# Performance work log

Hardware: AMD Instinct MI355X
Metric: run time of the kernel (lower is better)

The kernel has to match this reference:

```python
import jax, jax.numpy as jnp
import numpy as np

SCALAR_DIM = 64
VECTOR_DIM = 32
SPIN = 2
N_NODES = 50000
N_EDGES = 1600000
GEO_DIM = 3
IN_DIM = 2 * SCALAR_DIM + VECTOR_DIM + GEO_DIM  # 163
HID = SCALAR_DIM + VECTOR_DIM  # 96


def setup_inputs() -> dict:
    key = jax.random.key(0)
    ks = jax.random.split(key, 9)
    h_scalar = jax.random.normal(ks[0], (N_NODES, SCALAR_DIM), dtype=jnp.float32)
    h_vector = jax.random.normal(ks[1], (N_NODES, VECTOR_DIM), dtype=jnp.float32)
    edge_index = jax.random.randint(ks[2], (2, N_EDGES), 0, N_NODES, dtype=jnp.int64)
    pos = jax.random.normal(ks[3], (N_NODES, 2), dtype=jnp.float32)
    orientation = jax.random.uniform(ks[4], (N_NODES, 1), dtype=jnp.float32)
    # MLP params (Linear: y = x @ W.T + b; store as [in, out] for jnp)
    lim1 = 1.0 / np.sqrt(IN_DIM)
    lim2 = 1.0 / np.sqrt(HID)
    W1 = jax.random.uniform(ks[5], (IN_DIM, HID), minval=-lim1, maxval=lim1, dtype=jnp.float32)
    b1 = jax.random.uniform(ks[6], (HID,), minval=-lim1, maxval=lim1, dtype=jnp.float32)
    W2 = jax.random.uniform(ks[7], (HID, HID), minval=-lim2, maxval=lim2, dtype=jnp.float32)
    b2 = jax.random.uniform(ks[8], (HID,), minval=-lim2, maxval=lim2, dtype=jnp.float32)
    return dict(h_scalar=h_scalar, h_vector=h_vector, edge_index=edge_index,
                pos=pos, orientation=orientation, W1=W1, b1=b1, W2=W2, b2=b2)


def reference(h_scalar, h_vector, edge_index, pos, orientation, W1, b1, W2, b2):
    src, dst = edge_index[0], edge_index[1]
    delta_pos = pos[src] - pos[dst]                         # [E,2]
    dist = jnp.linalg.norm(delta_pos, axis=1, keepdims=True) + 1e-6  # [E,1]
    phi_global = jnp.arctan2(delta_pos[:, 1], delta_pos[:, 0])       # [E]
    alpha_i = orientation[dst, 0]                           # [E]
    delta_phi = phi_global - alpha_i
    geo_feat = jnp.concatenate([dist,
                                jnp.cos(SPIN * delta_phi)[:, None],
                                jnp.sin(SPIN * delta_phi)[:, None]], axis=-1)  # [E,3]
    beta_j = orientation[src, 0]
    rot_angle = (beta_j - alpha_i) * SPIN
    c, s = jnp.cos(rot_angle), jnp.sin(rot_angle)
    R = jnp.stack([jnp.stack([c, -s], -1), jnp.stack([s, c], -1)], axis=-2)  # [E,2,2]
    num_vecs = VECTOR_DIM // 2
    v_j = h_vector[src].reshape(-1, num_vecs, 2)            # [E,V/2,2]
    v_j_rot = jnp.einsum('eij,evj->evi', R, v_j).reshape(-1, VECTOR_DIM)
    msg_input = jnp.concatenate([h_scalar[src], h_scalar[dst], v_j_rot, geo_feat], axis=-1)
    h = jax.nn.silu(msg_input @ W1 + b1)
    raw_msg = h @ W2 + b2                                   # [E, S+V]
    msg_scalar = raw_msg[:, :SCALAR_DIM]
    msg_vector = raw_msg[:, SCALAR_DIM:]
    out_scalar = jax.ops.segment_sum(msg_scalar, dst, num_segments=N_NODES)
    out_vector = jax.ops.segment_sum(msg_vector, dst, num_segments=N_NODES)
    return h_scalar + out_scalar, h_vector + out_vector
```

## Files before the change

### kernel.cpp

```cpp
#include <hip/hip_runtime.h>
#include <hip/hip_bf16.h>

#define N_NODESC 50000
#define N_EDGESC 1600000
#define SDIM 64
#define VDIM 32
#define HID 96
#define IN_DIMC 163

#define GRID_E 6250
#define TPB_E 4
#define NXCD 8
#define XQ (GRID_E / NXCD)
#define XR (GRID_E % NXCD)

typedef float f32x4 __attribute__((ext_vector_type(4)));
typedef short s16x8 __attribute__((ext_vector_type(8)));

__device__ __forceinline__ float bf2f(__hip_bfloat16 x) { return __bfloat162float(x); }
__device__ __forceinline__ __hip_bfloat16 f2bf(float x) { return __float2bfloat16(x); }
__device__ __forceinline__ float bfbits2f(short b) {
    unsigned u = ((unsigned)(unsigned short)b) << 16;
    return __builtin_bit_cast(float, u);
}
__device__ __forceinline__ short f2bfbits(float x) {
    __hip_bfloat16 h = __float2bfloat16(x);
    return *(const short*)&h;
}

__global__ void detect_zero(const int* ei, int* flag, int* __restrict__ counts) {
    int i = blockIdx.x * blockDim.x + threadIdx.x;
    if (i < N_NODESC) counts[i] = 0;
    if (i == 0) {
        int z = 1;
        for (int k = 0; k < 64; ++k) {
            if (ei[2 * k + 1] != 0) { z = 0; break; }
        }
        *flag = z;
    }
}

__global__ void fused_init(const float* __restrict__ hs, const float* __restrict__ hv,
                           float* __restrict__ out, int* __restrict__ counts,
                           const float* __restrict__ W1, const float* __restrict__ W2,
                           __hip_bfloat16* __restrict__ SrcRec,
                           __hip_bfloat16* __restrict__ WbT2,
                           __hip_bfloat16* __restrict__ W1cgT,
                           __hip_bfloat16* __restrict__ W2Tb,
                           const int* __restrict__ ei, const int* __restrict__ flag64) {
    int i = blockIdx.x * blockDim.x + threadIdx.x;
    if (i < N_NODESC * (SDIM + VDIM))
        out[i] = (i < N_NODESC * SDIM) ? hs[i] : hv[i - N_NODESC * SDIM];
    if (i < N_NODESC * VDIM) {
        int n = i >> 5, f = i & 31;
        SrcRec[n * 128 + 96 + f] = f2bf(hv[i]);
    }
    if (i < 192 * 64) {
        int n = i >> 6, k = i & 63;
        float val = (n < 96) ? W1[k * HID + n] : W1[(64 + k) * HID + (n - 96)];
        WbT2[i] = f2bf(val);
    }
    if (i < 96 * 64) {
        int n = i >> 6, k = i & 63;
        float val = 0.f;
        if (k < 32) val = W1[(128 + k) * HID + n];
        else if (k < 35) val = W1[(160 + (k - 32)) * HID + n];
        W1cgT[i] = f2bf(val);
    }
    if (i < 96 * 96) {
        int n = i / 96, k = i - (i / 96) * 96;
        W2Tb[i] = f2bf(W2[k * HID + n]);
    }
    if (i < N_EDGESC) {
        int dN;
        if (*flag64) dN = (int)((const long long*)ei)[N_EDGESC + i];
        else dN = ei[N_EDGESC + i];
        atomicAdd(&counts[dN], 1);
    }
}

__global__ __launch_bounds__(256, 2) void node_precompute_mfma(
    const float* __restrict__ hs, const __hip_bfloat16* __restrict__ WbT2,
    const float* __restrict__ b1,
    __hip_bfloat16* __restrict__ SrcRec, __hip_bfloat16* __restrict__ Qt) {
    __shared__ __hip_bfloat16 sA[64][72];
    __shared__ __hip_bfloat16 sOut[64][200];
    const int t = threadIdx.x;
    const int lane = t & 63;
    const int w = t >> 6;
    const int m16 = lane & 15;
    const int q = lane >> 4;
    const int nb = blockIdx.x * 64;

    for (int idx = t; idx < 64 * 64; idx += 256) {
        int node = idx >> 6, f = idx & 63;
        int g = nb + node;
        sA[node][f] = f2bf(g < N_NODESC ? hs[g * SDIM + f] : 0.f);
    }
    __syncthreads();

    s16x8 bfr[3][2];
    float b1v[3];
    for (int nt = 0; nt < 3; ++nt) {
        int n_out = w * 48 + nt * 16 + m16;
        for (int kt = 0; kt < 2; ++kt)
            bfr[nt][kt] = *(const s16x8*)&WbT2[n_out * 64 + kt * 32 + q * 8];
        b1v[nt] = (n_out < 96) ? b1[n_out] : 0.f;
    }

    for (int ms = 0; ms < 4; ++ms) {
        s16x8 afr[2];
        for (int kt = 0; kt < 2; ++kt)
            afr[kt] = *(const s16x8*)&sA[ms * 16 + m16][kt * 32 + q * 8];
        f32x4 acc[3];
        for (int nt = 0; nt < 3; ++nt) acc[nt] = (f32x4){0.f, 0.f, 0.f, 0.f};
        for (int nt = 0; nt < 3; ++nt)
            for (int kt = 0; kt < 2; ++kt)
                acc[nt] = __builtin_amdgcn_mfma_f32_16x16x32_bf16(
                    afr[kt], bfr[nt][kt], acc[nt], 0, 0, 0);
        for (int nt = 0; nt < 3; ++nt) {
            int n_out = w * 48 + nt * 16 + m16;
            for (int r = 0; r < 4; ++r)
                sOut[ms * 16 + q * 4 + r][n_out] = f2bf(acc[nt][r] + b1v[nt]);
        }
    }
    __syncthreads();

    for (int idx = t; idx < 64 * 12; idx += 256) {
        int node = idx / 12, ch = idx - (idx / 12) * 12;
        int g = nb + node;
        if (g < N_NODESC)
            *(s16x8*)&SrcRec[g * 128 + ch * 8] = *(const s16x8*)&sOut[node][ch * 8];
    }
    for (int idx = t; idx < 64 * 12; idx += 256) {
        int node = idx / 12, ch = idx - (idx / 12) * 12;
        int g = nb + node;
        if (g < N_NODESC)
            *(s16x8*)&Qt[g * 96 + ch * 8] = *(const s16x8*)&sOut[node][96 + ch * 8];
    }
}

__global__ __launch_bounds__(1024) void scan_kernel(
    const int* __restrict__ counts, int* __restrict__ cur) {
    __shared__ int part[1024];
    const int t = threadIdx.x;
    const int CH = (N_NODESC + 1023) / 1024;
    int lo = t * CH;
    int hi = lo + CH; if (hi > N_NODESC) hi = N_NODESC;
    int s = 0;
    for (int i = lo; i < hi; ++i) s += counts[i];
    part[t] = s;
    __syncthreads();
    for (int d = 1; d < 1024; d <<= 1) {
        int v = (t >= d) ? part[t - d] : 0;
        __syncthreads();
        part[t] += v;
        __syncthreads();
    }
    int run = (t == 0) ? 0 : part[t - 1];
    for (int i = lo; i < hi; ++i) {
        int c = counts[i];
        cur[i] = run;
        run += c;
    }
}

__global__ __launch_bounds__(256) void scatter_kernel(
    const int* __restrict__ ei, const int* __restrict__ flag64,
    int* __restrict__ cur, int2* __restrict__ edges) {
    int e = blockIdx.x * blockDim.x + threadIdx.x;
    if (e >= N_EDGESC) return;
    int sN, dN;
    if (*flag64) {
        const long long* e64 = (const long long*)ei;
        sN = (int)e64[e]; dN = (int)e64[N_EDGESC + e];
    } else { sN = ei[e]; dN = ei[N_EDGESC + e]; }
    int p = atomicAdd(&cur[dN], 1);
    edges[p] = make_int2(sN, dN);
}

__global__ __launch_bounds__(256, 3) void edge_kernel_sorted(
    const int2* __restrict__ edges,
    const float* __restrict__ pos, const float* __restrict__ ori,
    const __hip_bfloat16* __restrict__ W2Tb, const float* __restrict__ b2,
    const __hip_bfloat16* __restrict__ SrcRec, const __hip_bfloat16* __restrict__ Qt,
    const __hip_bfloat16* __restrict__ W1cgT,
    float* __restrict__ out) {
    __shared__ int s_srcM[2][64], s_dstM[2][64];
    __shared__ alignas(16) __hip_bfloat16 hA[64][104];
    __shared__ alignas(16) __hip_bfloat16 s_vf[64][104];
    __shared__ alignas(16) short sW2f[18 * 64 * 8];
    __shared__ int s_segstart[66];

    const int t = threadIdx.x;
    const int lane = t & 63;
    const int w = t >> 6;
    const int m16 = lane & 15;
    const int q = lane >> 4;
    const int el = t >> 2;
    const int quad = t & 3;

    if (w == 0) {
        for (int f = 0; f < 18; ++f) {
            int nt = f / 3, kt = f - (f / 3) * 3;
            *(s16x8*)&sW2f[(f * 64 + lane) * 8] =
                *(const s16x8*)&W2Tb[(nt * 16 + m16) * 96 + kt * 32 + q * 8];
        }
    }
    s16x8 bfrC[6][2];
    #pragma unroll
    for (int nt = 0; nt < 6; ++nt)
        #pragma unroll
        for (int kt = 0; kt < 2; ++kt)
            bfrC[nt][kt] = *(const s16x8*)&W1cgT[(nt * 16 + m16) * 64 + kt * 32 + q * 8];
    float b2v[6];
    #pragma unroll
    for (int nt = 0; nt < 6; ++nt) b2v[nt] = b2[nt * 16 + m16];

    int b = blockIdx.x;
    int xcd = b & 7, bi = b >> 3;
    int c = (xcd < XR) ? (xcd * (XQ + 1) + bi)
                       : (XR * (XQ + 1) + (xcd - XR) * XQ + bi);
    const int tile0 = c * TPB_E;

    int2 edT1;
    s16x8 hvvT;
    float rcT, rsT;
    float gdT, gcgT, gsgT;
    {
        int2 edT = edges[tile0 * 64 + el];
        edT1 = edges[(tile0 + 1) * 64 + el];
        hvvT = *(const s16x8*)&SrcRec[edT.x * 128 + 96 + quad * 8];
        int sN = edT.x, dN = edT.y;
        float ca, sa, cb, sb;
        __sincosf(2.0f * ori[dN], &sa, &ca);
        __sincosf(2.0f * ori[sN], &sb, &cb);
        rcT = cb * ca + sb * sa;
        rsT = sb * ca - cb * sa;
        float dx = pos[2 * sN] - pos[2 * dN];
        float dy = pos[2 * sN + 1] - pos[2 * dN + 1];
        float d2 = dx * dx + dy * dy;
        gdT = sqrtf(d2) + 1e-6f;
        float c2f, s2f;
        if (d2 > 0.f) {
            float inv = 1.0f / d2;
            c2f = (dx * dx - dy * dy) * inv;
            s2f = 2.0f * dx * dy * inv;
        } else { c2f = 1.0f; s2f = 0.0f; }
        gcgT = c2f * ca + s2f * sa;
        gsgT = s2f * ca - c2f * sa;
        if (quad == 0) { s_srcM[0][el] = sN; s_dstM[0][el] = dN; }
    }
    __syncthreads();
    s16x8 pqP[3], pqQ[3];
    #pragma unroll
    for (int i2 = 0; i2 < 3; ++i2) {
        int item = i2 * 256 + t;
        int e = item / 12;
        int j = (item - e * 12) * 8;
        pqP[i2] = *(const s16x8*)&SrcRec[s_srcM[0][e] * 128 + j];
        pqQ[i2] = *(const s16x8*)&Qt[s_dstM[0][e] * 96 + j];
    }

    int cur = 0;
    for (int tl = 0; tl < TPB_E; ++tl) {
        const int nx = cur ^ 1;
        const int tlN2 = (tl + 2 < TPB_E) ? tl + 2 : TPB_E - 1;

        {
            s16x8 rv;
            #pragma unroll
            for (int p2 = 0; p2 < 4; ++p2) {
                float x = bfbits2f(hvvT[2 * p2]), y = bfbits2f(hvvT[2 * p2 + 1]);
                rv[2 * p2]     = f2bfbits(rcT * x - rsT * y);
                rv[2 * p2 + 1] = f2bfbits(rsT * x + rcT * y);
            }
            *(s16x8*)&hA[el][quad * 8] = rv;
            s16x8 up = (s16x8){0, 0, 0, 0, 0, 0, 0, 0};
            if (quad == 0) {
                up[0] = f2bfbits(gdT); up[1] = f2bfbits(gcgT); up[2] = f2bfbits(gsgT);
            }
            *(s16x8*)&hA[el][32 + quad * 8] = up;
        }
        int2 edT2 = edges[(tile0 + tlN2) * 64 + el];
        s16x8 hvvN = *(const s16x8*)&SrcRec[edT1.x * 128 + 96 + quad * 8];
        {
            s16x8 afr0 = *(const s16x8*)&hA[w * 16 + m16][q * 8];
            s16x8 afr1 = *(const s16x8*)&hA[w * 16 + m16][32 + q * 8];
            #pragma unroll
            for (int nt = 0; nt < 6; ++nt) {
                f32x4 a1 = __builtin_amdgcn_mfma_f32_16x16x32_bf16(
                    afr0, bfrC[nt][0], (f32x4){0.f, 0.f, 0.f, 0.f}, 0, 0, 0);
                a1 = __builtin_amdgcn_mfma_f32_16x16x32_bf16(
                    afr1, bfrC[nt][1], a1, 0, 0, 0);
                int u = nt * 16 + m16;
                #pragma unroll
                for (int r = 0; r < 4; ++r)
                    s_vf[w * 16 + q * 4 + r][u] = f2bf(a1[r]);
            }
        }
        float rcN, rsN, gdN, gcgN, gsgN;
        {
            int sN = edT1.x, dN = edT1.y;
            float ca, sa, cb, sb;
            __sincosf(2.0f * ori[dN], &sa, &ca);
            __sincosf(2.0f * ori[sN], &sb, &cb);
            rcN = cb * ca + sb * sa;
            rsN = sb * ca - cb * sa;
            float dx = pos[2 * sN] - pos[2 * dN];
            float dy = pos[2 * sN + 1] - pos[2 * dN + 1];
            float d2 = dx * dx + dy * dy;
            gdN = sqrtf(d2) + 1e-6f;
            float c2f, s2f;
            if (d2 > 0.f) {
                float inv = 1.0f / d2;
                c2f = (dx * dx - dy * dy) * inv;
                s2f = 2.0f * dx * dy * inv;
            } else { c2f = 1.0f; s2f = 0.0f; }
            gcgN = c2f * ca + s2f * sa;
            gsgN = s2f * ca - c2f * sa;
            if (quad == 0) { s_srcM[nx][el] = sN; s_dstM[nx][el] = dN; }
        }
        __syncthreads();

        #pragma unroll
        for (int i2 = 0; i2 < 3; ++i2) {
            int item = i2 * 256 + t;
            int e = item / 12;
            int j = (item - e * 12) * 8;
            s16x8 Vv = *(const s16x8*)&s_vf[e][j];
            s16x8 hb;
            #pragma unroll
            for (int k2 = 0; k2 < 8; ++k2) {
                float pre = bfbits2f(pqP[i2][k2]) + bfbits2f(pqQ[i2][k2])
                          + bfbits2f(Vv[k2]);
                float h = pre / (1.0f + __expf(-pre));
                hb[k2] = f2bfbits(h);
            }
            *(s16x8*)&hA[e][j] = hb;
        }
        __syncthreads();

        #pragma unroll
        for (int i2 = 0; i2 < 3; ++i2) {
            int item = i2 * 256 + t;
            int e = item / 12;
            int j = (item - e * 12) * 8;
            pqP[i2] = *(const s16x8*)&SrcRec[s_srcM[nx][e] * 128 + j];
            pqQ[i2] = *(const s16x8*)&Qt[s_dstM[nx][e] * 96 + j];
        }
        {
            s16x8 afr[3];
            #pragma unroll
            for (int kt = 0; kt < 3; ++kt)
                afr[kt] = *(const s16x8*)&hA[w * 16 + m16][kt * 32 + q * 8];
            f32x4 acc[6];
            #pragma unroll
            for (int nt = 0; nt < 6; ++nt) acc[nt] = (f32x4){0.f, 0.f, 0.f, 0.f};
            #pragma unroll
            for (int nt = 0; nt < 6; ++nt)
                #pragma unroll
                for (int kt = 0; kt < 3; ++kt) {
                    s16x8 bf = *(const s16x8*)&sW2f[((nt * 3 + kt) * 64 + lane) * 8];
                    acc[nt] = __builtin_amdgcn_mfma_f32_16x16x32_bf16(
                        afr[kt], bf, acc[nt], 0, 0, 0);
                }
            #pragma unroll
            for (int nt = 0; nt < 6; ++nt) {
                int u = nt * 16 + m16;
                float bb = b2v[nt];
                #pragma unroll
                for (int r = 0; r < 4; ++r)
                    s_vf[w * 16 + q * 4 + r][u] = f2bf(acc[nt][r] + bb);
            }
        }
        __syncthreads();

        {
            int dl = s_dstM[cur][lane];
            int dp = (lane > 0) ? s_dstM[cur][lane - 1] : -1;
            bool bnd = (lane > 0) && (dl != dp);
            unsigned long long mask = __ballot(bnd);
            int nseg = (int)__popcll(mask) + 1;
            if (bnd) s_segstart[__popcll(mask & (~0ull >> (63 - lane)))] = lane;
            if (lane == 0) s_segstart[0] = 0;

            for (int idx = t; idx < nseg * HID; idx += 256) {
                int sg = idx / HID;
                int u = idx - sg * HID;
                int e0 = s_segstart[sg];
                int e1 = (sg + 1 < nseg) ? s_segstart[sg + 1] : 64;
                float sum = 0.f;
                for (int e = e0; e < e1; ++e) sum += bf2f(s_vf[e][u]);
                int dN = s_dstM[cur][e0];
                if (u < SDIM) atomicAdd(&out[dN * SDIM + u], sum);
                else atomicAdd(&out[N_NODESC * SDIM + dN * VDIM + (u - SDIM)], sum);
            }
        }

        edT1 = edT2; hvvT = hvvN;
        rcT = rcN; rsT = rsN; gdT = gdN; gcgT = gcgN; gsgT = gsgN;
        cur = nx;
        __syncthreads();
    }
}

__global__ __launch_bounds__(128) void node_precompute(
    const float* __restrict__ hs, const float* __restrict__ hv,
    const float* __restrict__ W1, const float* __restrict__ b1,
    __hip_bfloat16* __restrict__ Pp, __hip_bfloat16* __restrict__ Qt,
    __hip_bfloat16* __restrict__ Ut, __hip_bfloat16* __restrict__ Vt) {
    int n = blockIdx.x;
    __shared__ float s_hs[SDIM];
    __shared__ float s_hv[VDIM];
    int t = threadIdx.x;
    if (t < 64) s_hs[t] = hs[n * SDIM + t];
    else if (t < 96) s_hv[t - 64] = hv[n * VDIM + (t - 64)];
    __syncthreads();
    if (t < HID) {
        float p = b1[t], qq = 0.f, u = 0.f, v = 0.f;
        for (int k = 0; k < 64; ++k) {
            float x = s_hs[k];
            p += x * W1[k * HID + t];
            qq += x * W1[(64 + k) * HID + t];
        }
        for (int pr = 0; pr < 16; ++pr) {
            float x = s_hv[2 * pr], y = s_hv[2 * pr + 1];
            float wa = W1[(128 + 2 * pr) * HID + t];
            float wb = W1[(128 + 2 * pr + 1) * HID + t];
            u += x * wa + y * wb;
            v += x * wb - y * wa;
        }
        Pp[n * HID + t] = f2bf(p);
        Qt[n * HID + t] = f2bf(qq);
        Ut[n * HID + t] = f2bf(u);
        Vt[n * HID + t] = f2bf(v);
    }
}

__global__ void init_out(const float* __restrict__ hs, const float* __restrict__ hv,
                         float* __restrict__ out) {
    int i = blockIdx.x * blockDim.x + threadIdx.x;
    if (i >= N_NODESC * (SDIM + VDIM)) return;
    out[i] = (i < N_NODESC * SDIM) ? hs[i] : hv[i - N_NODESC * SDIM];
}

__global__ void detect_kernel(const int* ei, int* flag) {
    if (blockIdx.x == 0 && threadIdx.x == 0) {
        int z = 1;
        for (int k = 0; k < 64; ++k) {
            if (ei[2 * k + 1] != 0) { z = 0; break; }
        }
        *flag = z;
    }
}

__global__ __launch_bounds__(256) void edge_kernel(
    const int* __restrict__ ei, const float* __restrict__ pos,
    const float* __restrict__ ori, const float* __restrict__ W1,
    const float* __restrict__ W2, const float* __restrict__ b2,
    const __hip_bfloat16* __restrict__ Pp, const __hip_bfloat16* __restrict__ Qt,
    const __hip_bfloat16* __restrict__ Ut, const __hip_bfloat16* __restrict__ Vt,
    const int* __restrict__ flag64, float* __restrict__ out) {
    __shared__ int s_src[64], s_dst[64];
    __shared__ float s_c[64], s_s[64], s_d[64], s_cg[64], s_sg[64];
    __shared__ float s_w1d[3][HID];
    __shared__ __hip_bfloat16 hA[64][104];
    __shared__ __hip_bfloat16 W2T[HID][104];

    const int t = threadIdx.x;
    const int lane = t & 63;
    const int w = t >> 6;
    const int m16 = lane & 15;
    const int q = lane >> 4;

    for (int idx = t; idx < HID * HID; idx += 256) {
        int k = idx / HID;
        int n = idx - k * HID;
        W2T[n][k] = f2bf(W2[idx]);
    }
    for (int idx = t; idx < 3 * HID; idx += 256) {
        int r = idx / HID, j = idx - r * HID;
        s_w1d[r][j] = W1[(160 + r) * HID + j];
    }
    __syncthreads();

    s16x8 bfr[6][3];
    for (int nt = 0; nt < 6; ++nt)
        for (int kt = 0; kt < 3; ++kt)
            bfr[nt][kt] = *(const s16x8*)&W2T[nt * 16 + m16][kt * 32 + q * 8];
    float b2v[6];
    for (int nt = 0; nt < 6; ++nt) b2v[nt] = b2[nt * 16 + m16];

    const bool i64 = (*flag64 != 0);
    const long long* ei64 = (const long long*)ei;

    for (int tile = blockIdx.x; tile < N_EDGESC / 64; tile += gridDim.x) {
        __syncthreads();

        if (t < 64) {
            int e = tile * 64 + t;
            int sN, dN;
            if (i64) { sN = (int)ei64[e]; dN = (int)ei64[N_EDGESC + e]; }
            else     { sN = ei[e];        dN = ei[N_EDGESC + e]; }
            s_src[t] = sN; s_dst[t] = dN;
            float ca, sa, cb, sb;
            __sincosf(2.0f * ori[dN], &sa, &ca);
            __sincosf(2.0f * ori[sN], &sb, &cb);
            s_c[t] = cb * ca + sb * sa;
            s_s[t] = sb * ca - cb * sa;
            float dx = pos[2 * sN] - pos[2 * dN];
            float dy = pos[2 * sN + 1] - pos[2 * dN + 1];
            float d2 = dx * dx + dy * dy;
            s_d[t] = sqrtf(d2) + 1e-6f;
            float c2f, s2f;
            if (d2 > 0.f) {
                float inv = 1.0f / d2;
                c2f = (dx * dx - dy * dy) * inv;
                s2f = 2.0f * dx * dy * inv;
            } else { c2f = 1.0f; s2f = 0.0f; }
            s_cg[t] = c2f * ca + s2f * sa;
            s_sg[t] = s2f * ca - c2f * sa;
        }
        __syncthreads();

        for (int p = 0; p < 24; ++p) {
            int idx = p * 256 + t;
            int e = idx / HID;
            int j = idx - e * HID;
            int sN = s_src[e], dN = s_dst[e];
            float pre = bf2f(Pp[sN * HID + j]) + bf2f(Qt[dN * HID + j])
                      + s_c[e] * bf2f(Ut[sN * HID + j])
                      + s_s[e] * bf2f(Vt[sN * HID + j])
                      + s_d[e] * s_w1d[0][j] + s_cg[e] * s_w1d[1][j]
                      + s_sg[e] * s_w1d[2][j];
            float h = pre / (1.0f + __expf(-pre));
            hA[e][j] = f2bf(h);
        }
        __syncthreads();

        f32x4 acc[6];
        for (int nt = 0; nt < 6; ++nt) acc[nt] = (f32x4){0.f, 0.f, 0.f, 0.f};
        s16x8 afr[3];
        for (int kt = 0; kt < 3; ++kt)
            afr[kt] = *(const s16x8*)&hA[w * 16 + m16][kt * 32 + q * 8];
        for (int nt = 0; nt < 6; ++nt)
            for (int kt = 0; kt < 3; ++kt)
                acc[nt] = __builtin_amdgcn_mfma_f32_16x16x32_bf16(
                    afr[kt], bfr[nt][kt], acc[nt], 0, 0, 0);

        for (int nt = 0; nt < 6; ++nt) {
            int u = nt * 16 + m16;
            for (int r = 0; r < 4; ++r) {
                int eloc = w * 16 + q * 4 + r;
                int dN = s_dst[eloc];
                float val = acc[nt][r] + b2v[nt];
                if (u < SDIM) atomicAdd(&out[dN * SDIM + u], val);
                else atomicAdd(&out[N_NODESC * SDIM + dN * VDIM + (u - SDIM)], val);
            }
        }
    }
}

__global__ __launch_bounds__(192) void edge_fallback(
    const int* __restrict__ ei, const float* __restrict__ hs,
    const float* __restrict__ hv, const float* __restrict__ pos,
    const float* __restrict__ ori, const float* __restrict__ W1,
    const float* __restrict__ b1, const float* __restrict__ W2,
    const float* __restrict__ b2, const int* __restrict__ flag64,
    float* __restrict__ out) {
    __shared__ float s_msg[IN_DIMC];
    __shared__ float s_h[HID];
    int e = blockIdx.x;
    int t = threadIdx.x;
    const bool i64 = (*flag64 != 0);
    int sN, dN;
    if (i64) {
        const long long* e64 = (const long long*)ei;
        sN = (int)e64[e]; dN = (int)e64[N_EDGESC + e];
    } else { sN = ei[e]; dN = ei[N_EDGESC + e]; }

    if (t < IN_DIMC) {
        if (t < 64) s_msg[t] = hs[sN * SDIM + t];
        else if (t < 128) s_msg[t] = hs[dN * SDIM + (t - 64)];
        else {
            float ca, sa, cb, sb;
            __sincosf(2.0f * ori[dN], &sa, &ca);
            __sincosf(2.0f * ori[sN], &sb, &cb);
            float c = cb * ca + sb * sa;
            float s = sb * ca - cb * sa;
            float dx = pos[2 * sN] - pos[2 * dN];
            float dy = pos[2 * sN + 1] - pos[2 * dN + 1];
            float d2 = dx * dx + dy * dy;
            if (t < 160) {
                int pr = (t - 128) >> 1;
                float x = hv[sN * VDIM + 2 * pr], y = hv[sN * VDIM + 2 * pr + 1];
                s_msg[t] = ((t & 1) == 0) ? (c * x - s * y) : (s * x + c * y);
            } else if (t == 160) s_msg[t] = sqrtf(d2) + 1e-6f;
            else {
                float c2f = 1.0f, s2f = 0.0f;
                if (d2 > 0.f) {
                    float inv = 1.0f / d2;
                    c2f = (dx * dx - dy * dy) * inv;
                    s2f = 2.0f * dx * dy * inv;
                }
                s_msg[t] = (t == 161) ? (c2f * ca + s2f * sa) : (s2f * ca - c2f * sa);
            }
        }
    }
    __syncthreads();
    if (t < HID) {
        float a = b1[t];
        for (int k = 0; k < IN_DIMC; ++k) a += s_msg[k] * W1[k * HID + t];
        s_h[t] = a / (1.0f + __expf(-a));
    }
    __syncthreads();
    if (t < HID) {
        float a = b2[t];
        for (int k = 0; k < HID; ++k) a += s_h[k] * W2[k * HID + t];
        if (t < SDIM) atomicAdd(&out[dN * SDIM + t], a);
        else atomicAdd(&out[N_NODESC * SDIM + dN * VDIM + (t - SDIM)], a);
    }
}

extern "C" void kernel_launch(void* const* d_in, const int* in_sizes, int n_in,
                              void* d_out, int out_size, void* d_ws, size_t ws_size,
                              hipStream_t stream) {
    const float* hs  = (const float*)d_in[0];
    const float* hv  = (const float*)d_in[1];
    const int*   ei  = (const int*)d_in[2];
    const float* pos = (const float*)d_in[3];
    const float* ori = (const float*)d_in[4];
    const float* W1  = (const float*)d_in[5];
    const float* b1  = (const float*)d_in[6];
    const float* W2  = (const float*)d_in[7];
    const float* b2  = (const float*)d_in[8];
    float* out = (float*)d_out;

    const size_t SREC = (size_t)N_NODESC * 128 * sizeof(__hip_bfloat16);
    const size_t QTB  = (size_t)N_NODESC * 96 * sizeof(__hip_bfloat16);
    const size_t CNT  = ((size_t)N_NODESC * sizeof(int) + 255) & ~255ull;
    const size_t EDG  = (size_t)N_EDGESC * sizeof(int2);
    const size_t WBT2 = ((size_t)192 * 64 * 2 + 255) & ~255ull;
    const size_t W1CG = ((size_t)96 * 64 * 2 + 255) & ~255ull;
    const size_t W2TS = ((size_t)96 * 96 * 2 + 255) & ~255ull;
    const size_t SORT_WS = SREC + QTB + 2 * CNT + EDG + WBT2 + W1CG + W2TS + 256;

    const size_t TBL = (size_t)N_NODESC * HID * sizeof(__hip_bfloat16);
    const bool big = ws_size >= 4 * TBL + 16;
    const bool srt = ws_size >= SORT_WS;

    if (srt) {
        char* ws = (char*)d_ws;
        __hip_bfloat16* SrcRec = (__hip_bfloat16*)(ws);
        __hip_bfloat16* Qt     = (__hip_bfloat16*)(ws + SREC);
        int* counts            = (int*)(ws + SREC + QTB);
        int* cur               = (int*)(ws + SREC + QTB + CNT);
        int2* edges            = (int2*)(ws + SREC + QTB + 2 * CNT);
        __hip_bfloat16* WbT2   = (__hip_bfloat16*)(ws + SREC + QTB + 2 * CNT + EDG);
        __hip_bfloat16* W1cgT  = (__hip_bfloat16*)(ws + SREC + QTB + 2 * CNT + EDG + WBT2);
        __hip_bfloat16* W2Tb   = (__hip_bfloat16*)(ws + SREC + QTB + 2 * CNT + EDG + WBT2 + W1CG);
        int* flag              = (int*)(ws + SREC + QTB + 2 * CNT + EDG + WBT2 + W1CG + W2TS);

        detect_zero<<<(N_NODESC + 255) / 256, 256, 0, stream>>>(ei, flag, counts);
        fused_init<<<(N_NODESC * (SDIM + VDIM) + 255) / 256, 256, 0, stream>>>(
            hs, hv, out, counts, W1, W2, SrcRec, WbT2, W1cgT, W2Tb, ei, flag);
        scan_kernel<<<1, 1024, 0, stream>>>(counts, cur);
        scatter_kernel<<<N_EDGESC / 256, 256, 0, stream>>>(ei, flag, cur, edges);
        node_precompute_mfma<<<(N_NODESC + 63) / 64, 256, 0, stream>>>(
            hs, WbT2, b1, SrcRec, Qt);
        edge_kernel_sorted<<<GRID_E, 256, 0, stream>>>(edges, pos, ori, W2Tb, b2,
                                                       SrcRec, Qt, W1cgT, out);
    } else if (big) {
        char* ws = (char*)d_ws;
        __hip_bfloat16* Pp = (__hip_bfloat16*)(ws);
        __hip_bfloat16* Qt = (__hip_bfloat16*)(ws + TBL);
        __hip_bfloat16* Ut = (__hip_bfloat16*)(ws + 2 * TBL);
        __hip_bfloat16* Vt = (__hip_bfloat16*)(ws + 3 * TBL);
        int* flag = (int*)(ws + 4 * TBL);
        init_out<<<(N_NODESC * (SDIM + VDIM) + 255) / 256, 256, 0, stream>>>(hs, hv, out);
        detect_kernel<<<1, 64, 0, stream>>>(ei, flag);
        node_precompute<<<N_NODESC, 128, 0, stream>>>(hs, hv, W1, b1, Pp, Qt, Ut, Vt);
        edge_kernel<<<2500, 256, 0, stream>>>(ei, pos, ori, W1, W2, b2,
                                              Pp, Qt, Ut, Vt, flag, out);
    } else {
        int* flag = (int*)d_ws;
        init_out<<<(N_NODESC * (SDIM + VDIM) + 255) / 256, 256, 0, stream>>>(hs, hv, out);
        detect_kernel<<<1, 64, 0, stream>>>(ei, flag);
        edge_fallback<<<N_EDGESC, 192, 0, stream>>>(ei, hs, hv, pos, ori, W1, b1,
                                                    W2, b2, flag, out);
    }
}
```

Baseline: 607.1 us.

## Compute hidden activations in MFMA fragment layout, drop two barriers; vectorize init

The edge kernel now has each lane gather the P/Q rows and compute the SiLU hidden activations directly in the A-fragment layout used by the second MFMA. This removes the round trip through shared memory and the two __syncthreads per tile that surrounded it. The init kernel is also vectorized with float4 copies and 8-wide bf16 packing, and its grid is shrunk to exactly cover the edge count. In exchange, the gathers become less coalesced because each lane reads its own edge row per fragment.

```diff
diff --git a/kernel.cpp b/kernel.cpp
--- a/kernel.cpp
+++ b/kernel.cpp
@@ -49,11 +49,22 @@
                            __hip_bfloat16* __restrict__ W2Tb,
                            const int* __restrict__ ei, const int* __restrict__ flag64) {
     int i = blockIdx.x * blockDim.x + threadIdx.x;
-    if (i < N_NODESC * (SDIM + VDIM))
-        out[i] = (i < N_NODESC * SDIM) ? hs[i] : hv[i - N_NODESC * SDIM];
-    if (i < N_NODESC * VDIM) {
-        int n = i >> 5, f = i & 31;
-        SrcRec[n * 128 + 96 + f] = f2bf(hv[i]);
+    if (i < N_NODESC * (SDIM + VDIM) / 4) {
+        const int HS4 = N_NODESC * SDIM / 4;
+        float4 v = (i < HS4) ? ((const float4*)hs)[i] : ((const float4*)hv)[i - HS4];
+        ((float4*)out)[i] = v;
+    }
+    if (i < N_NODESC * VDIM / 8) {
+        int n = i >> 2, c = i & 3;
+        const float4* hv4 = (const float4*)hv;
+        float4 a = hv4[n * 8 + c * 2];
+        float4 bq = hv4[n * 8 + c * 2 + 1];
+        s16x8 o;
+        o[0] = f2bfbits(a.x);  o[1] = f2bfbits(a.y);
+        o[2] = f2bfbits(a.z);  o[3] = f2bfbits(a.w);
+        o[4] = f2bfbits(bq.x); o[5] = f2bfbits(bq.y);
+        o[6] = f2bfbits(bq.z); o[7] = f2bfbits(bq.w);
+        *(s16x8*)&SrcRec[n * 128 + 96 + c * 8] = o;
     }
     if (i < 192 * 64) {
         int n = i >> 6, k = i & 63;
@@ -71,7 +82,7 @@
         int n = i / 96, k = i - (i / 96) * 96;
         W2Tb[i] = f2bf(W2[k * HID + n]);
     }
-    if (i < N_EDGESC) {
+    {
         int dN;
         if (*flag64) dN = (int)((const long long*)ei)[N_EDGESC + i];
         else dN = ei[N_EDGESC + i];
@@ -187,7 +198,7 @@
     const __hip_bfloat16* __restrict__ W1cgT,
     float* __restrict__ out) {
     __shared__ int s_srcM[2][64], s_dstM[2][64];
-    __shared__ alignas(16) __hip_bfloat16 hA[64][104];
+    __shared__ alignas(16) __hip_bfloat16 hVG[64][72];
     __shared__ alignas(16) __hip_bfloat16 s_vf[64][104];
     __shared__ alignas(16) short sW2f[18 * 64 * 8];
     __shared__ int s_segstart[66];
@@ -199,6 +210,7 @@
     const int q = lane >> 4;
     const int el = t >> 2;
     const int quad = t & 3;
+    const int eM = w * 16 + m16;
 
     if (w == 0) {
         for (int f = 0; f < 18; ++f) {
@@ -253,13 +265,13 @@
     }
     __syncthreads();
     s16x8 pqP[3], pqQ[3];
-    #pragma unroll
-    for (int i2 = 0; i2 < 3; ++i2) {
-        int item = i2 * 256 + t;
-        int e = item / 12;
-        int j = (item - e * 12) * 8;
-        pqP[i2] = *(const s16x8*)&SrcRec[s_srcM[0][e] * 128 + j];
-        pqQ[i2] = *(const s16x8*)&Qt[s_dstM[0][e] * 96 + j];
+    {
+        int sN = s_srcM[0][eM], dN = s_dstM[0][eM];
+        #pragma unroll
+        for (int kt = 0; kt < 3; ++kt) {
+            pqP[kt] = *(const s16x8*)&SrcRec[sN * 128 + kt * 32 + q * 8];
+            pqQ[kt] = *(const s16x8*)&Qt[dN * 96 + kt * 32 + q * 8];
+        }
     }
 
     int cur = 0;
@@ -275,18 +287,18 @@
                 rv[2 * p2]     = f2bfbits(rcT * x - rsT * y);
                 rv[2 * p2 + 1] = f2bfbits(rsT * x + rcT * y);
             }
-            *(s16x8*)&hA[el][quad * 8] = rv;
+            *(s16x8*)&hVG[el][quad * 8] = rv;
             s16x8 up = (s16x8){0, 0, 0, 0, 0, 0, 0, 0};
             if (quad == 0) {
                 up[0] = f2bfbits(gdT); up[1] = f2bfbits(gcgT); up[2] = f2bfbits(gsgT);
             }
-            *(s16x8*)&hA[el][32 + quad * 8] = up;
+            *(s16x8*)&hVG[el][32 + quad * 8] = up;
         }
         int2 edT2 = edges[(tile0 + tlN2) * 64 + el];
         s16x8 hvvN = *(const s16x8*)&SrcRec[edT1.x * 128 + 96 + quad * 8];
         {
-            s16x8 afr0 = *(const s16x8*)&hA[w * 16 + m16][q * 8];
-            s16x8 afr1 = *(const s16x8*)&hA[w * 16 + m16][32 + q * 8];
+            s16x8 afr0 = *(const s16x8*)&hVG[eM][q * 8];
+            s16x8 afr1 = *(const s16x8*)&hVG[eM][32 + q * 8];
             #pragma unroll
             for (int nt = 0; nt < 6; ++nt) {
                 f32x4 a1 = __builtin_amdgcn_mfma_f32_16x16x32_bf16(
@@ -321,39 +333,31 @@
             gsgN = s2f * ca - c2f * sa;
             if (quad == 0) { s_srcM[nx][el] = sN; s_dstM[nx][el] = dN; }
         }
-        __syncthreads();
-
+
+        s16x8 afr[3];
         #pragma unroll
-        for (int i2 = 0; i2 < 3; ++i2) {
-            int item = i2 * 256 + t;
-            int e = item / 12;
-            int j = (item - e * 12) * 8;
-            s16x8 Vv = *(const s16x8*)&s_vf[e][j];
+        for (int kt = 0; kt < 3; ++kt) {
+            int j = kt * 32 + q * 8;
+            s16x8 Vv = *(const s16x8*)&s_vf[eM][j];
             s16x8 hb;
             #pragma unroll
             for (int k2 = 0; k2 < 8; ++k2) {
-                float pre = bfbits2f(pqP[i2][k2]) + bfbits2f(pqQ[i2][k2])
+                float pre = bfbits2f(pqP[kt][k2]) + bfbits2f(pqQ[kt][k2])
                           + bfbits2f(Vv[k2]);
                 float h = pre / (1.0f + __expf(-pre));
                 hb[k2] = f2bfbits(h);
             }
-            *(s16x8*)&hA[e][j] = hb;
-        }
-        __syncthreads();
-
-        #pragma unroll
-        for (int i2 = 0; i2 < 3; ++i2) {
-            int item = i2 * 256 + t;
-            int e = item / 12;
-            int j = (item - e * 12) * 8;
-            pqP[i2] = *(const s16x8*)&SrcRec[s_srcM[nx][e] * 128 + j];
-            pqQ[i2] = *(const s16x8*)&Qt[s_dstM[nx][e] * 96 + j];
+            afr[kt] = hb;
         }
         {
-            s16x8 afr[3];
+            int sN = s_srcM[nx][eM], dN = s_dstM[nx][eM];
             #pragma unroll
-            for (int kt = 0; kt < 3; ++kt)
-                afr[kt] = *(const s16x8*)&hA[w * 16 + m16][kt * 32 + q * 8];
+            for (int kt = 0; kt < 3; ++kt) {
+                pqP[kt] = *(const s16x8*)&SrcRec[sN * 128 + kt * 32 + q * 8];
+                pqQ[kt] = *(const s16x8*)&Qt[dN * 96 + kt * 32 + q * 8];
+            }
+        }
+        {
             f32x4 acc[6];
             #pragma unroll
             for (int nt = 0; nt < 6; ++nt) acc[nt] = (f32x4){0.f, 0.f, 0.f, 0.f};
@@ -663,7 +667,7 @@
         int* flag              = (int*)(ws + SREC + QTB + 2 * CNT + EDG + WBT2 + W1CG + W2TS);
 
         detect_zero<<<(N_NODESC + 255) / 256, 256, 0, stream>>>(ei, flag, counts);
-        fused_init<<<(N_NODESC * (SDIM + VDIM) + 255) / 256, 256, 0, stream>>>(
+        fused_init<<<N_EDGESC / 256, 256, 0, stream>>>(
             hs, hv, out, counts, W1, W2, SrcRec, WbT2, W1cgT, W2Tb, ei, flag);
         scan_kernel<<<1, 1024, 0, stream>>>(counts, cur);
         scatter_kernel<<<N_EDGESC / 256, 256, 0, stream>>>(ei, flag, cur, edges);
```

Result: faster. 589.5 us (-2.9%).
